# Performance work log

Measured on AMD Instinct MI355X. Metric: run time of the kernel, lower is better.

Reference implementation:

```python
import jax, jax.numpy as jnp
import numpy as np

RES = 7          # pooler resolution
RATIO = 2        # sampling ratio
LEVEL_STRIDES = (4, 8, 16, 32)
NUM_CLASSES = 4
BINS = 8
EPS = 1e-5


def roi_align_one(feat, boxes, scale):
    """feat: [C,H,W]; boxes: [N,4] (t,l,b,r) in image coords. Returns [N,C,RES,RES]."""
    C, H, W = feat.shape
    P = RES * RATIO
    t = boxes[:, 0] * scale - 0.5
    l = boxes[:, 1] * scale - 0.5
    b = boxes[:, 2] * scale - 0.5
    r = boxes[:, 3] * scale - 0.5
    bin_h = (b - t) / RES
    bin_w = (r - l) / RES
    grid = (jnp.arange(P, dtype=feat.dtype) + 0.5) / RATIO      # [P] bin-unit offsets
    ys = jnp.clip(t[:, None] + bin_h[:, None] * grid, 0.0, H - 1.0)  # [N,P]
    xs = jnp.clip(l[:, None] + bin_w[:, None] * grid, 0.0, W - 1.0)  # [N,P]
    y0 = jnp.floor(ys).astype(jnp.int32)
    x0 = jnp.floor(xs).astype(jnp.int32)
    y1 = jnp.minimum(y0 + 1, H - 1)
    x1 = jnp.minimum(x0 + 1, W - 1)
    wy = (ys - y0.astype(feat.dtype))[:, :, None]   # [N,P,1]
    wx = (xs - x0.astype(feat.dtype))[:, None, :]   # [N,1,P]

    def g(yi, xi):  # -> [C,N,P,P]
        return feat[:, yi[:, :, None], xi[:, None, :]]

    v = (g(y0, x0) * (1 - wy) * (1 - wx) + g(y0, x1) * (1 - wy) * wx
         + g(y1, x0) * wy * (1 - wx) + g(y1, x1) * wy * wx)      # [C,N,P,P]
    v = v.reshape(C, -1, RES, RATIO, RES, RATIO).mean(axis=(3, 5))  # avg-pool bins
    return jnp.transpose(v, (1, 0, 2, 3))


def setup_inputs():
    key = jax.random.key(0)
    ks = jax.random.split(key, 16)
    B, N, C, FC = 2, 256, 256, 1024
    f0 = jax.random.normal(ks[0], (B, C, 128, 128), jnp.float32)
    f1 = jax.random.normal(ks[1], (B, C, 64, 64), jnp.float32)
    f2 = jax.random.normal(ks[2], (B, C, 32, 32), jnp.float32)
    f3 = jax.random.normal(ks[3], (B, C, 16, 16), jnp.float32)
    yx = jax.random.uniform(ks[4], (B, N, 2), jnp.float32) * 384.0 + 64.0
    hw = jax.random.uniform(ks[5], (B, N, 2), jnp.float32) * 96.0 + 32.0
    bbox2d = jnp.concatenate([yx, hw], axis=-1)            # yxhw
    anchor_id = jax.random.randint(ks[6], (B, N, 1), 0, 12, jnp.int32)
    zeropad = (jax.random.uniform(ks[7], (B, N, 1)) > 0.1).astype(jnp.float32)
    in_dim = C * RES * RES
    fc1_w = jax.random.normal(ks[8], (FC, in_dim), jnp.float32) / np.sqrt(in_dim)
    fc2_w = jax.random.normal(ks[9], (FC, FC), jnp.float32) / np.sqrt(FC)
    out_ch = NUM_CLASSES * (1 + 6 + 2 * BINS) + 1           # 93
    pred_w = jax.random.normal(ks[10], (out_ch, FC), jnp.float32) * 0.01
    return dict(f0=f0, f1=f1, f2=f2, f3=f3, bbox2d=bbox2d, anchor_id=anchor_id,
                zeropad=zeropad,
                fc1_w=fc1_w, fc1_b=jnp.zeros((FC,)), bn1_g=jnp.ones((FC,)), bn1_b=jnp.zeros((FC,)),
                fc2_w=fc2_w, fc2_b=jnp.zeros((FC,)), bn2_g=jnp.ones((FC,)), bn2_b=jnp.zeros((FC,)),
                pred_w=pred_w, pred_b=jnp.zeros((out_ch,)))


def reference(f0, f1, f2, f3, bbox2d, anchor_id, zeropad,
              fc1_w, fc1_b, bn1_g, bn1_b, fc2_w, fc2_b, bn2_g, bn2_b, pred_w, pred_b):
    feats = [f0, f1, f2, f3]
    B, N, _ = bbox2d.shape
    y, x, h, w = [bbox2d[..., i] for i in range(4)]
    tlbr = jnp.stack([y - h / 2, x - w / 2, y + h / 2, x + w / 2], axis=-1)  # [B,N,4]
    level = anchor_id[..., 0] // 3                                          # [B,N]

    # Route each proposal to its FPN level: compute roi-align per level, select by mask.
    pooled = 0.0
    for i, stride in enumerate(LEVEL_STRIDES):
        roi = jax.vmap(lambda f, bx, s=stride: roi_align_one(f, bx, 1.0 / s))(feats[i], tlbr)  # [B,N,C,R,R]
        mask = (level == i).astype(roi.dtype)[..., None, None, None]
        pooled = pooled + roi * mask

    xflat = pooled.reshape(B * N, -1)
    for w_, b_, g_, be_ in [(fc1_w, fc1_b, bn1_g, bn1_b), (fc2_w, fc2_b, bn2_g, bn2_b)]:
        xflat = xflat @ w_.T + b_
        mu = xflat.mean(axis=0)
        var = xflat.var(axis=0)
        xflat = (xflat - mu) * jax.lax.rsqrt(var + EPS) * g_ + be_   # BatchNorm1d (train mode)
        xflat = jax.nn.relu(xflat)
    pred = (xflat @ pred_w.T + pred_b).reshape(B, N, -1) * zeropad    # [B,N,93]
    strides = level.astype(pred.dtype)[..., None] * zeropad           # [B,N,1]

    # decode: slice per-loss channels (category: NC+1; others: NC*dims)
    ctgr_logit = pred[..., 0:NUM_CLASSES + 1]                                  # [B,N,5]
    d3 = pred[..., 5:5 + NUM_CLASSES * 6].reshape(B, N, NUM_CLASSES, 6)
    o = 5 + NUM_CLASSES * 6
    yaw_cls = pred[..., o:o + NUM_CLASSES * BINS].reshape(B, N, NUM_CLASSES, BINS)
    o += NUM_CLASSES * BINS
    yaw_res = pred[..., o:o + NUM_CLASSES * BINS].reshape(B, N, NUM_CLASSES, BINS)

    # apply 3d box deltas per class (vectorized over class dim)
    anc = bbox2d[:, :, None, :]                     # [B,N,1,4] yxhw
    st = 4.0 * jnp.exp2(strides)                    # [B,N,1] anchor stride in px
    cy = anc[..., 0] + d3[..., 0] * anc[..., 2]
    cx = anc[..., 1] + d3[..., 1] * anc[..., 3]
    nh = anc[..., 2] * jnp.exp(d3[..., 2])
    nw = anc[..., 3] * jnp.exp(d3[..., 3])
    z = d3[..., 4] * st
    ln = jnp.exp(d3[..., 5]) * st
    bbox3d = jnp.stack([cy, cx, z, nh, nw, ln], axis=-1)  # [B,N,NC,6]

    out = jnp.concatenate([
        bbox3d.reshape(B, N, -1),                         # 24
        jax.nn.softmax(ctgr_logit, axis=-1),              # 5
        jax.nn.softmax(yaw_cls, axis=-1).reshape(B, N, -1),  # 32
        (jax.nn.sigmoid(yaw_res) * 0.6 - 0.3).reshape(B, N, -1),  # 32
    ], axis=-1)                                           # [B,N,93]
    return out
```

## Files before the change

kernel.cpp:

```cpp
#include <hip/hip_runtime.h>
#include <cstdint>
#include <cstddef>

typedef __attribute__((ext_vector_type(8))) short bf16x8;
typedef __attribute__((ext_vector_type(4))) float f32x4;
typedef __attribute__((ext_vector_type(4))) int   i32x4;

#define C_CH   256
#define NBOX   512
#define FCDIM  1024
#define K1     12544
#define OUTC   93

__device__ __forceinline__ unsigned short f2bf(float f) {
    unsigned u = __float_as_uint(f);
    u += 0x7fffu + ((u >> 16) & 1u);
    return (unsigned short)(u >> 16);
}
__device__ __forceinline__ float bf2f(short s) {
    return __uint_as_float((unsigned)(unsigned short)s << 16);
}

__global__ __launch_bounds__(256) void cast_bf16_kernel(
    const float* __restrict__ in, short* __restrict__ out, int n8)
{
    int i = blockIdx.x * 256 + threadIdx.x;
    if (i >= n8) return;
    const float4* p = (const float4*)(in + (size_t)i * 8);
    float4 a = p[0], b = p[1];
    union { unsigned short s[8]; i32x4 v; } u;
    u.s[0] = f2bf(a.x); u.s[1] = f2bf(a.y); u.s[2] = f2bf(a.z); u.s[3] = f2bf(a.w);
    u.s[4] = f2bf(b.x); u.s[5] = f2bf(b.y); u.s[6] = f2bf(b.z); u.s[7] = f2bf(b.w);
    *(i32x4*)(out + (size_t)i * 8) = u.v;
}

__global__ __launch_bounds__(256) void transpose_cl_kernel(
    const float* __restrict__ in, short* __restrict__ out, int HW)
{
    __shared__ short tile[128 * 66];
    int p0 = blockIdx.x * 128;
    int c0 = blockIdx.y * 64;
    int b  = blockIdx.z;
    const float* src = in + ((size_t)b * C_CH + c0) * HW + p0;
    int t = threadIdx.x;
    #pragma unroll
    for (int it = 0; it < 16; ++it) {
        int slot = it * 256 + t;
        int cl = slot >> 6;
        int pp = slot & 63;
        float2 v = *(const float2*)(src + (size_t)cl * HW + pp * 2);
        tile[(pp * 2) * 66 + cl]     = (short)f2bf(v.x);
        tile[(pp * 2 + 1) * 66 + cl] = (short)f2bf(v.y);
    }
    __syncthreads();
    short* dst = out + ((size_t)b * HW + p0) * C_CH + c0;
    #pragma unroll
    for (int it = 0; it < 16; ++it) {
        int pl = it * 8 + (t >> 5);
        int c2 = (t & 31) * 2;
        *(unsigned*)(dst + (size_t)pl * C_CH + c2) = *(const unsigned*)&tile[pl * 66 + c2];
    }
}

__global__ __launch_bounds__(512) void roi_kernel(
    const short* __restrict__ g0, const short* __restrict__ g1,
    const short* __restrict__ g2, const short* __restrict__ g3,
    const float* __restrict__ bbox, const int* __restrict__ aid,
    short* __restrict__ pooled)
{
    int bn  = blockIdx.x;
    int b   = bn >> 8;
    int t   = threadIdx.x;
    int c   = t & 255;
    int sub = t >> 8;

    __shared__ int   xo0[14], xo1[14];
    __shared__ float wxs[14];
    __shared__ int   yo0[14], yo1[14];
    __shared__ float wys[14];
    __shared__ short otile[K1];

    float yb = bbox[bn*4+0], xb = bbox[bn*4+1], hb = bbox[bn*4+2], wb = bbox[bn*4+3];
    int level = aid[bn] / 3;
    const short* gsrc = (level == 0) ? g0 : (level == 1) ? g1 : (level == 2) ? g2 : g3;
    int H = 128 >> level;
    float scale = 1.0f / (float)(4 << level);
    const short* gp = gsrc + (size_t)b * H * H * C_CH;

    if (t < 14) {
        float g  = ((float)t + 0.5f) * 0.5f;
        float l0 = (xb - 0.5f*wb) * scale - 0.5f;
        float bw = wb * scale * (1.0f/7.0f);
        float v  = fminf(fmaxf(l0 + bw * g, 0.0f), (float)(H-1));
        int i0 = (int)v;
        xo0[t] = i0 * C_CH;
        xo1[t] = min(i0 + 1, H - 1) * C_CH;
        wxs[t] = v - (float)i0;
    } else if (t < 28) {
        int sy = t - 14;
        float g  = ((float)sy + 0.5f) * 0.5f;
        float t0 = (yb - 0.5f*hb) * scale - 0.5f;
        float bh = hb * scale * (1.0f/7.0f);
        float v  = fminf(fmaxf(t0 + bh * g, 0.0f), (float)(H-1));
        int i0 = (int)v;
        yo0[sy] = i0 * H * C_CH;
        yo1[sy] = min(i0 + 1, H - 1) * H * C_CH;
        wys[sy] = v - (float)i0;
    }
    __syncthreads();

    #pragma unroll 2
    for (int s = sub; s < 49; s += 2) {
        int py = s / 7, px = s - py * 7;
        float acc = 0.0f;
        #pragma unroll
        for (int i = 0; i < 2; i++) {
            int sy = 2 * py + i;
            int ry0 = yo0[sy], ry1 = yo1[sy];
            float wy = wys[sy];
            #pragma unroll
            for (int j = 0; j < 2; j++) {
                int sx = 2 * px + j;
                int cx0 = xo0[sx] + c, cx1 = xo1[sx] + c;
                float wx = wxs[sx];
                float v00 = bf2f(gp[ry0 + cx0]);
                float v01 = bf2f(gp[ry0 + cx1]);
                float v10 = bf2f(gp[ry1 + cx0]);
                float v11 = bf2f(gp[ry1 + cx1]);
                float top = v00 * (1.0f - wx) + v01 * wx;
                float bot = v10 * (1.0f - wx) + v11 * wx;
                acc += top * (1.0f - wy) + bot * wy;
            }
        }
        otile[c * 49 + s] = (short)f2bf(acc * 0.25f);
    }
    __syncthreads();

    const i32x4* srcv = (const i32x4*)otile;
    i32x4* dstv = (i32x4*)(pooled + (size_t)bn * K1);
    for (int j = t; j < (K1 * 2) / 16; j += 512)
        dstv[j] = srcv[j];
}

__global__ __launch_bounds__(256) void gemm_mfma(
    const short* __restrict__ A, const short* __restrict__ Bt,
    float* __restrict__ part, int K, int KC)
{
    __shared__ short As[128 * 32];
    __shared__ short Bs[128 * 32];
    int t = threadIdx.x, lane = t & 63, w = t >> 6;
    int m0 = blockIdx.y * 128, n0 = blockIdx.x * 128;
    size_t k0 = (size_t)blockIdx.z * KC;

    int srow = t >> 1, scol = (t & 1) * 16;
    const short* pa = A  + (size_t)(m0 + srow) * K + scol + k0;
    const short* pb = Bt + (size_t)(n0 + srow) * K + scol + k0;
    short* wa = &As[srow * 32 + scol];
    short* wb = &Bs[srow * 32 + scol];

    int wr = (w >> 1) * 64, wc = (w & 1) * 64;
    int fr = lane & 15, kg = lane >> 4;
    const short* raf = &As[(wr + fr) * 32 + kg * 8];
    const short* rbf = &Bs[(wc + fr) * 32 + kg * 8];

    int nsteps = KC >> 5;
    i32x4 rA0 = *(const i32x4*)pa, rA1 = *(const i32x4*)(pa + 8);
    i32x4 rB0 = *(const i32x4*)pb, rB1 = *(const i32x4*)(pb + 8);

    f32x4 acc[4][4] = {};
    for (int s = 0; s < nsteps; ++s) {
        *(i32x4*)wa = rA0; *(i32x4*)(wa + 8) = rA1;
        *(i32x4*)wb = rB0; *(i32x4*)(wb + 8) = rB1;
        __syncthreads();
        if (s + 1 < nsteps) {
            const short* na = pa + (size_t)(s + 1) * 32;
            const short* nb = pb + (size_t)(s + 1) * 32;
            rA0 = *(const i32x4*)na; rA1 = *(const i32x4*)(na + 8);
            rB0 = *(const i32x4*)nb; rB1 = *(const i32x4*)(nb + 8);
        }
        bf16x8 af[4], bm[4];
        #pragma unroll
        for (int i = 0; i < 4; i++) af[i] = *(const bf16x8*)(raf + i * 16 * 32);
        #pragma unroll
        for (int j = 0; j < 4; j++) bm[j] = *(const bf16x8*)(rbf + j * 16 * 32);
        #pragma unroll
        for (int i = 0; i < 4; i++)
            #pragma unroll
            for (int j = 0; j < 4; j++)
                acc[i][j] = __builtin_amdgcn_mfma_f32_16x16x32_bf16(af[i], bm[j], acc[i][j], 0, 0, 0);
        __syncthreads();
    }

    float* base = part + (size_t)blockIdx.z * NBOX * FCDIM;
    #pragma unroll
    for (int i = 0; i < 4; i++)
        #pragma unroll
        for (int j = 0; j < 4; j++)
            #pragma unroll
            for (int r = 0; r < 4; r++) {
                int row = m0 + wr + i * 16 + kg * 4 + r;
                int col = n0 + wc + j * 16 + fr;
                base[(size_t)row * FCDIM + col] = acc[i][j][r];
            }
}

template<int NZ>
__global__ __launch_bounds__(256) void bn_stats1(
    const float* __restrict__ part, float* __restrict__ xsum, float* __restrict__ pstat)
{
    int tc = threadIdx.x & 63;
    int tr = threadIdx.x >> 6;
    int c  = blockIdx.x * 64 + tc;
    int r0 = blockIdx.y * 32;
    const size_t P = (size_t)NBOX * FCDIM;

    float s = 0.0f, q = 0.0f;
    #pragma unroll
    for (int rr = 0; rr < 8; rr++) {
        size_t o = (size_t)(r0 + tr + rr * 4) * FCDIM + c;
        float x = 0.0f;
        #pragma unroll
        for (int z = 0; z < NZ; z++) x += part[o + (size_t)z * P];
        xsum[o] = x;
        s += x; q += x * x;
    }
    __shared__ float Ss[4][64], Sq[4][64];
    Ss[tr][tc] = s; Sq[tr][tc] = q;
    __syncthreads();
    if (tr == 0) {
        float S = Ss[0][tc] + Ss[1][tc] + Ss[2][tc] + Ss[3][tc];
        float Q = Sq[0][tc] + Sq[1][tc] + Sq[2][tc] + Sq[3][tc];
        pstat[blockIdx.y * FCDIM + c] = S;
        pstat[16 * FCDIM + blockIdx.y * FCDIM + c] = Q;
    }
}

__global__ __launch_bounds__(256) void bn_stats2(
    const float* __restrict__ pstat, const float* __restrict__ g,
    const float* __restrict__ be, float* __restrict__ scsh)
{
    int c = blockIdx.x * 256 + threadIdx.x;
    float S = 0.0f, Q = 0.0f;
    #pragma unroll
    for (int i = 0; i < 16; i++) {
        S += pstat[i * FCDIM + c];
        Q += pstat[16 * FCDIM + i * FCDIM + c];
    }
    float mu  = S * (1.0f / NBOX);
    float var = Q * (1.0f / NBOX) - mu * mu;
    float a = g[c] * rsqrtf(var + 1e-5f);
    scsh[c]         = a;
    scsh[FCDIM + c] = be[c] - mu * a;
}

template<bool BF>
__global__ __launch_bounds__(256) void bn_apply(
    const float* __restrict__ xsum, const float* __restrict__ scsh,
    short* __restrict__ obf, float* __restrict__ of)
{
    size_t base = ((size_t)blockIdx.x * 256 + threadIdx.x) * 8;
    int c0 = (int)(base & (FCDIM - 1));
    float4 x0 = *(const float4*)(xsum + base);
    float4 x1 = *(const float4*)(xsum + base + 4);
    float4 a0 = *(const float4*)(scsh + c0);
    float4 a1 = *(const float4*)(scsh + c0 + 4);
    float4 b0 = *(const float4*)(scsh + FCDIM + c0);
    float4 b1 = *(const float4*)(scsh + FCDIM + c0 + 4);
    float r[8];
    r[0] = fmaxf(x0.x*a0.x + b0.x, 0.0f);
    r[1] = fmaxf(x0.y*a0.y + b0.y, 0.0f);
    r[2] = fmaxf(x0.z*a0.z + b0.z, 0.0f);
    r[3] = fmaxf(x0.w*a0.w + b0.w, 0.0f);
    r[4] = fmaxf(x1.x*a1.x + b1.x, 0.0f);
    r[5] = fmaxf(x1.y*a1.y + b1.y, 0.0f);
    r[6] = fmaxf(x1.z*a1.z + b1.z, 0.0f);
    r[7] = fmaxf(x1.w*a1.w + b1.w, 0.0f);
    if (BF) {
        union { unsigned short s[8]; i32x4 v; } u;
        #pragma unroll
        for (int i = 0; i < 8; i++) u.s[i] = f2bf(r[i]);
        *(i32x4*)(obf + base) = u.v;
    } else {
        *(float4*)(of + base)     = *(float4*)&r[0];
        *(float4*)(of + base + 4) = *(float4*)&r[4];
    }
}

__global__ __launch_bounds__(128) void pred_kernel(
    const float* __restrict__ xin, const float* __restrict__ pw,
    const float* __restrict__ pb, const float* __restrict__ bbox,
    const int* __restrict__ aid, const float* __restrict__ zp,
    float* __restrict__ out)
{
    int bn = blockIdx.x;
    int t  = threadIdx.x;
    __shared__ float xs[FCDIM];
    __shared__ float pr[OUTC];
    for (int i = t; i < FCDIM; i += 128)
        xs[i] = xin[(size_t)bn * FCDIM + i];
    __syncthreads();

    float z = zp[bn];
    if (t < OUTC) {
        const float* wrow = pw + (size_t)t * FCDIM;
        float acc = 0.0f;
        for (int k = 0; k < FCDIM; k += 4) {
            float4 w4 = *(const float4*)(wrow + k);
            acc += xs[k] * w4.x + xs[k+1] * w4.y + xs[k+2] * w4.z + xs[k+3] * w4.w;
        }
        pr[t] = (acc + pb[t]) * z;
    }
    __syncthreads();

    if (t < OUTC) {
        float y = bbox[bn*4+0], x = bbox[bn*4+1], h = bbox[bn*4+2], w = bbox[bn*4+3];
        int lvl = aid[bn] / 3;
        float st = 4.0f * exp2f((float)lvl * z);
        float o;
        if (t < 24) {
            int k = t / 6, j = t - k * 6;
            const float* d = &pr[5 + k * 6];
            switch (j) {
                case 0:  o = y + d[0] * h;  break;
                case 1:  o = x + d[1] * w;  break;
                case 2:  o = d[4] * st;     break;
                case 3:  o = h * expf(d[2]); break;
                case 4:  o = w * expf(d[3]); break;
                default: o = expf(d[5]) * st; break;
            }
        } else if (t < 29) {
            float m = pr[0];
            #pragma unroll
            for (int i = 1; i < 5; i++) m = fmaxf(m, pr[i]);
            float den = 0.0f;
            #pragma unroll
            for (int i = 0; i < 5; i++) den += expf(pr[i] - m);
            o = expf(pr[t - 24] - m) / den;
        } else if (t < 61) {
            int i = t - 29, k = i >> 3;
            const float* qq = &pr[29 + k * 8];
            float m = qq[0];
            #pragma unroll
            for (int ii = 1; ii < 8; ii++) m = fmaxf(m, qq[ii]);
            float den = 0.0f;
            #pragma unroll
            for (int ii = 0; ii < 8; ii++) den += expf(qq[ii] - m);
            o = expf(pr[t] - m) / den;
        } else {
            o = 1.0f / (1.0f + expf(-pr[t])) * 0.6f - 0.3f;
        }
        out[(size_t)bn * OUTC + t] = o;
    }
}

extern "C" void kernel_launch(void* const* d_in, const int* in_sizes, int n_in,
                              void* d_out, int out_size, void* d_ws, size_t ws_size,
                              hipStream_t stream)
{
    const float* f0   = (const float*)d_in[0];
    const float* f1   = (const float*)d_in[1];
    const float* f2   = (const float*)d_in[2];
    const float* f3   = (const float*)d_in[3];
    const float* bbox = (const float*)d_in[4];
    const int*   aid  = (const int*)d_in[5];
    const float* zp   = (const float*)d_in[6];
    const float* fc1w = (const float*)d_in[7];
    const float* bn1g = (const float*)d_in[9];
    const float* bn1b = (const float*)d_in[10];
    const float* fc2w = (const float*)d_in[11];
    const float* bn2g = (const float*)d_in[13];
    const float* bn2b = (const float*)d_in[14];
    const float* pw   = (const float*)d_in[15];
    const float* pb   = (const float*)d_in[16];
    float* out = (float*)d_out;

    char* ws = (char*)d_ws;
    short* pooled = (short*)(ws);
    float* xsum   = (float*)(ws);
    short* x1n    = (short*)(ws + 2097152);
    short* w2     = (short*)(ws + 3145728);
    float* x2n    = (float*)(ws + 5242880);
    short* gt0    = (short*)(ws + 12845056);
    short* gt1    = (short*)(ws + 29622272);
    short* gt2    = (short*)(ws + 33816576);
    short* gt3    = (short*)(ws + 34865152);
    short* w1     = (short*)(ws + 12845056);
    float* part2  = (float*)(ws + 12845056);
    float* part1  = (float*)(ws + 38535168);
    float* pstat  = (float*)(ws + 53215232);
    float* scsh   = (float*)(ws + 53346304);

    transpose_cl_kernel<<<dim3(128, 4, 2), 256, 0, stream>>>(f0, gt0, 16384);
    transpose_cl_kernel<<<dim3( 32, 4, 2), 256, 0, stream>>>(f1, gt1,  4096);
    transpose_cl_kernel<<<dim3(  8, 4, 2), 256, 0, stream>>>(f2, gt2,  1024);
    transpose_cl_kernel<<<dim3(  2, 4, 2), 256, 0, stream>>>(f3, gt3,   256);

    roi_kernel<<<NBOX, 512, 0, stream>>>(gt0, gt1, gt2, gt3, bbox, aid, pooled);

    cast_bf16_kernel<<<(K1 * FCDIM / 8 + 255) / 256, 256, 0, stream>>>(fc1w, w1, K1 * FCDIM / 8);

    dim3 g1(FCDIM / 128, NBOX / 128, 7);
    gemm_mfma<<<g1, 256, 0, stream>>>(pooled, w1, part1, K1, K1 / 7);

    cast_bf16_kernel<<<(FCDIM * FCDIM / 8 + 255) / 256, 256, 0, stream>>>(fc2w, w2, FCDIM * FCDIM / 8);

    bn_stats1<7><<<dim3(16, 16), 256, 0, stream>>>(part1, xsum, pstat);
    bn_stats2<<<4, 256, 0, stream>>>(pstat, bn1g, bn1b, scsh);
    bn_apply<true><<<256, 256, 0, stream>>>(xsum, scsh, x1n, nullptr);

    dim3 g2(FCDIM / 128, NBOX / 128, 8);
    gemm_mfma<<<g2, 256, 0, stream>>>(x1n, w2, part2, FCDIM, FCDIM / 8);

    bn_stats1<8><<<dim3(16, 16), 256, 0, stream>>>(part2, xsum, pstat);
    bn_stats2<<<4, 256, 0, stream>>>(pstat, bn2g, bn2b, scsh);
    bn_apply<false><<<256, 256, 0, stream>>>(xsum, scsh, nullptr, x2n);

    pred_kernel<<<NBOX, 128, 0, stream>>>(x2n, pw, pb, bbox, aid, zp, out);
}
```

Measured before the change: 152.5 us.

## Fuse fc1 weight cast into GEMM, merge transposes, retile fc1 to 256x256

Removes the separate fp32-to-bf16 cast pass over the large fc1 weight: a new fc1 GEMM reads fp32 weights directly and converts them to bf16 while staging into shared memory. It uses 256x256 tiles with 512 threads and split-K 14, replacing 128x128 tiles with split-K 7. The four per-level feature transposes are merged into one launch, and the workspace is re-laid out so the buffers no longer alias. The cost is twice the bytes read for the weight inside the GEMM, in-loop conversion work, higher register pressure from 32 accumulators per thread, and a larger split-K partial buffer for the BN stats to reduce.

```diff
diff --git a/kernel.cpp b/kernel.cpp
--- a/kernel.cpp
+++ b/kernel.cpp
@@ -11,6 +11,8 @@
 #define FCDIM  1024
 #define K1     12544
 #define OUTC   93
+#define Z1     14
+#define Z2     8
 
 __device__ __forceinline__ unsigned short f2bf(float f) {
     unsigned u = __float_as_uint(f);
@@ -34,31 +36,41 @@
     *(i32x4*)(out + (size_t)i * 8) = u.v;
 }
 
-__global__ __launch_bounds__(256) void transpose_cl_kernel(
-    const float* __restrict__ in, short* __restrict__ out, int HW)
+__global__ __launch_bounds__(256) void transpose_all_kernel(
+    const float* __restrict__ f0, const float* __restrict__ f1,
+    const float* __restrict__ f2, const float* __restrict__ f3,
+    short* __restrict__ g0, short* __restrict__ g1,
+    short* __restrict__ g2, short* __restrict__ g3)
 {
     __shared__ short tile[128 * 66];
-    int p0 = blockIdx.x * 128;
-    int c0 = blockIdx.y * 64;
-    int b  = blockIdx.z;
-    const float* src = in + ((size_t)b * C_CH + c0) * HW + p0;
+    int id = blockIdx.x;
+    const float* src; short* dst; int HW, nx;
+    if (id < 1024)      { src = f0; dst = g0; HW = 16384; nx = 128; }
+    else if (id < 1280) { id -= 1024; src = f1; dst = g1; HW = 4096; nx = 32; }
+    else if (id < 1344) { id -= 1280; src = f2; dst = g2; HW = 1024; nx = 8; }
+    else                { id -= 1344; src = f3; dst = g3; HW = 256;  nx = 2; }
+    int xb = id % nx;  int rest = id / nx;
+    int cy = rest & 3; int b = rest >> 2;
+    int p0 = xb * 128, c0 = cy * 64;
+
+    const float* s = src + ((size_t)b * C_CH + c0) * HW + p0;
     int t = threadIdx.x;
     #pragma unroll
     for (int it = 0; it < 16; ++it) {
         int slot = it * 256 + t;
         int cl = slot >> 6;
         int pp = slot & 63;
-        float2 v = *(const float2*)(src + (size_t)cl * HW + pp * 2);
+        float2 v = *(const float2*)(s + (size_t)cl * HW + pp * 2);
         tile[(pp * 2) * 66 + cl]     = (short)f2bf(v.x);
         tile[(pp * 2 + 1) * 66 + cl] = (short)f2bf(v.y);
     }
     __syncthreads();
-    short* dst = out + ((size_t)b * HW + p0) * C_CH + c0;
+    short* d = dst + ((size_t)b * HW + p0) * C_CH + c0;
     #pragma unroll
     for (int it = 0; it < 16; ++it) {
         int pl = it * 8 + (t >> 5);
         int c2 = (t & 31) * 2;
-        *(unsigned*)(dst + (size_t)pl * C_CH + c2) = *(const unsigned*)&tile[pl * 66 + c2];
+        *(unsigned*)(d + (size_t)pl * C_CH + c2) = *(const unsigned*)&tile[pl * 66 + c2];
     }
 }
 
@@ -142,6 +154,75 @@
         dstv[j] = srcv[j];
 }
 
+__global__ __launch_bounds__(512, 2) void gemm_fc1(
+    const short* __restrict__ A, const float* __restrict__ Bw,
+    float* __restrict__ part, int K, int KC)
+{
+    __shared__ short As[256 * 32];
+    __shared__ short Bs[256 * 32];
+    int t = threadIdx.x, lane = t & 63, w = t >> 6;
+    int n0 = blockIdx.x * 256, m0 = blockIdx.y * 256;
+    size_t k0 = (size_t)blockIdx.z * KC;
+
+    int srow = t >> 1, scol = (t & 1) * 16;
+    const short* pa  = A  + (size_t)(m0 + srow) * K + scol + k0;
+    const float* pbw = Bw + (size_t)(n0 + srow) * K + scol + k0;
+    short* wa = &As[srow * 32 + scol];
+    short* wb = &Bs[srow * 32 + scol];
+
+    int wr = (w >> 2) * 128, wc = (w & 3) * 64;
+    int fr = lane & 15, kg = lane >> 4;
+    const short* raf = &As[(wr + fr) * 32 + kg * 8];
+    const short* rbf = &Bs[(wc + fr) * 32 + kg * 8];
+
+    int nsteps = KC >> 5;
+    i32x4  rA0 = *(const i32x4*)pa,        rA1 = *(const i32x4*)(pa + 8);
+    float4 rB0 = *(const float4*)pbw,      rB1 = *(const float4*)(pbw + 4);
+    float4 rB2 = *(const float4*)(pbw + 8), rB3 = *(const float4*)(pbw + 12);
+
+    f32x4 acc[8][4] = {};
+    for (int s = 0; s < nsteps; ++s) {
+        union { unsigned short us[16]; i32x4 v[2]; } ub;
+        ub.us[0]  = f2bf(rB0.x); ub.us[1]  = f2bf(rB0.y); ub.us[2]  = f2bf(rB0.z); ub.us[3]  = f2bf(rB0.w);
+        ub.us[4]  = f2bf(rB1.x); ub.us[5]  = f2bf(rB1.y); ub.us[6]  = f2bf(rB1.z); ub.us[7]  = f2bf(rB1.w);
+        ub.us[8]  = f2bf(rB2.x); ub.us[9]  = f2bf(rB2.y); ub.us[10] = f2bf(rB2.z); ub.us[11] = f2bf(rB2.w);
+        ub.us[12] = f2bf(rB3.x); ub.us[13] = f2bf(rB3.y); ub.us[14] = f2bf(rB3.z); ub.us[15] = f2bf(rB3.w);
+        *(i32x4*)wa = rA0;     *(i32x4*)(wa + 8) = rA1;
+        *(i32x4*)wb = ub.v[0]; *(i32x4*)(wb + 8) = ub.v[1];
+        __syncthreads();
+        if (s + 1 < nsteps) {
+            const short* na = pa  + (size_t)(s + 1) * 32;
+            const float* nb = pbw + (size_t)(s + 1) * 32;
+            rA0 = *(const i32x4*)na;       rA1 = *(const i32x4*)(na + 8);
+            rB0 = *(const float4*)nb;      rB1 = *(const float4*)(nb + 4);
+            rB2 = *(const float4*)(nb + 8); rB3 = *(const float4*)(nb + 12);
+        }
+        bf16x8 af[8], bm[4];
+        #pragma unroll
+        for (int i = 0; i < 8; i++) af[i] = *(const bf16x8*)(raf + i * 16 * 32);
+        #pragma unroll
+        for (int j = 0; j < 4; j++) bm[j] = *(const bf16x8*)(rbf + j * 16 * 32);
+        #pragma unroll
+        for (int i = 0; i < 8; i++)
+            #pragma unroll
+            for (int j = 0; j < 4; j++)
+                acc[i][j] = __builtin_amdgcn_mfma_f32_16x16x32_bf16(af[i], bm[j], acc[i][j], 0, 0, 0);
+        __syncthreads();
+    }
+
+    float* base = part + (size_t)blockIdx.z * NBOX * FCDIM;
+    #pragma unroll
+    for (int i = 0; i < 8; i++)
+        #pragma unroll
+        for (int j = 0; j < 4; j++)
+            #pragma unroll
+            for (int r = 0; r < 4; r++) {
+                int row = m0 + wr + i * 16 + kg * 4 + r;
+                int col = n0 + wc + j * 16 + fr;
+                base[(size_t)row * FCDIM + col] = acc[i][j][r];
+            }
+}
+
 __global__ __launch_bounds__(256) void gemm_mfma(
     const short* __restrict__ A, const short* __restrict__ Bt,
     float* __restrict__ part, int K, int KC)
@@ -376,42 +457,36 @@
 
     char* ws = (char*)d_ws;
     short* pooled = (short*)(ws);
-    float* xsum   = (float*)(ws);
-    short* x1n    = (short*)(ws + 2097152);
-    short* w2     = (short*)(ws + 3145728);
-    float* x2n    = (float*)(ws + 5242880);
-    short* gt0    = (short*)(ws + 12845056);
-    short* gt1    = (short*)(ws + 29622272);
-    short* gt2    = (short*)(ws + 33816576);
-    short* gt3    = (short*)(ws + 34865152);
-    short* w1     = (short*)(ws + 12845056);
-    float* part2  = (float*)(ws + 12845056);
-    float* part1  = (float*)(ws + 38535168);
-    float* pstat  = (float*)(ws + 53215232);
-    float* scsh   = (float*)(ws + 53346304);
-
-    transpose_cl_kernel<<<dim3(128, 4, 2), 256, 0, stream>>>(f0, gt0, 16384);
-    transpose_cl_kernel<<<dim3( 32, 4, 2), 256, 0, stream>>>(f1, gt1,  4096);
-    transpose_cl_kernel<<<dim3(  8, 4, 2), 256, 0, stream>>>(f2, gt2,  1024);
-    transpose_cl_kernel<<<dim3(  2, 4, 2), 256, 0, stream>>>(f3, gt3,   256);
+    short* gt0    = (short*)(ws + 13631488);
+    short* gt1    = (short*)(ws + 30408704);
+    short* gt2    = (short*)(ws + 34603008);
+    short* gt3    = (short*)(ws + 35651584);
+    short* w2     = (short*)(ws + 36700160);
+    float* part1  = (float*)(ws + 40894464);
+    float* part2  = (float*)(ws + 71303168);
+    float* xsum   = (float*)(ws + 89128960);
+    short* x1n    = (short*)(ws + 91226112);
+    float* x2n    = (float*)(ws + 92274688);
+    float* pstat  = (float*)(ws + 94371840);
+    float* scsh   = (float*)(ws + 94502912);
+
+    transpose_all_kernel<<<1360, 256, 0, stream>>>(f0, f1, f2, f3, gt0, gt1, gt2, gt3);
 
     roi_kernel<<<NBOX, 512, 0, stream>>>(gt0, gt1, gt2, gt3, bbox, aid, pooled);
 
-    cast_bf16_kernel<<<(K1 * FCDIM / 8 + 255) / 256, 256, 0, stream>>>(fc1w, w1, K1 * FCDIM / 8);
-
-    dim3 g1(FCDIM / 128, NBOX / 128, 7);
-    gemm_mfma<<<g1, 256, 0, stream>>>(pooled, w1, part1, K1, K1 / 7);
+    dim3 g1(FCDIM / 256, NBOX / 256, Z1);
+    gemm_fc1<<<g1, 512, 0, stream>>>(pooled, fc1w, part1, K1, K1 / Z1);
 
     cast_bf16_kernel<<<(FCDIM * FCDIM / 8 + 255) / 256, 256, 0, stream>>>(fc2w, w2, FCDIM * FCDIM / 8);
 
-    bn_stats1<7><<<dim3(16, 16), 256, 0, stream>>>(part1, xsum, pstat);
+    bn_stats1<Z1><<<dim3(16, 16), 256, 0, stream>>>(part1, xsum, pstat);
     bn_stats2<<<4, 256, 0, stream>>>(pstat, bn1g, bn1b, scsh);
     bn_apply<true><<<256, 256, 0, stream>>>(xsum, scsh, x1n, nullptr);
 
-    dim3 g2(FCDIM / 128, NBOX / 128, 8);
-    gemm_mfma<<<g2, 256, 0, stream>>>(x1n, w2, part2, FCDIM, FCDIM / 8);
-
-    bn_stats1<8><<<dim3(16, 16), 256, 0, stream>>>(part2, xsum, pstat);
+    dim3 g2(FCDIM / 128, NBOX / 128, Z2);
+    gemm_mfma<<<g2, 256, 0, stream>>>(x1n, w2, part2, FCDIM, FCDIM / Z2);
+
+    bn_stats1<Z2><<<dim3(16, 16), 256, 0, stream>>>(part2, xsum, pstat);
     bn_stats2<<<4, 256, 0, stream>>>(pstat, bn2g, bn2b, scsh);
     bn_apply<false><<<256, 256, 0, stream>>>(xsum, scsh, nullptr, x2n);
 
```

After: 154.6 us. About the same (+1.4%).

## Double-buffer GEMM via direct global-to-LDS loads, merge transposes, deepen split-K

Applied to the files above, without the earlier changes.

Replaces the register-staged GEMM with a double-buffered version that uses global_load_lds to copy tiles straight into shared memory while the current tile feeds MFMA. FC1 split-K grows from 7 to 14 slices for more blocks, and blocks are indexed linearly so that blocks with the same row tile run together. The four per-level transpose launches are merged into one launch, and the workspace is re-laid out so buffers no longer alias. In exchange, more split-K partials must be written and reduced, and the workspace footprint is larger.

```diff
diff --git a/kernel.cpp b/kernel.cpp
--- a/kernel.cpp
+++ b/kernel.cpp
@@ -11,6 +11,8 @@
 #define FCDIM  1024
 #define K1     12544
 #define OUTC   93
+#define Z1     14
+#define Z2     8
 
 __device__ __forceinline__ unsigned short f2bf(float f) {
     unsigned u = __float_as_uint(f);
@@ -19,6 +21,11 @@
 }
 __device__ __forceinline__ float bf2f(short s) {
     return __uint_as_float((unsigned)(unsigned short)s << 16);
+}
+__device__ __forceinline__ void stage16(const short* g, const short* l) {
+    __builtin_amdgcn_global_load_lds(
+        (const __attribute__((address_space(1))) void*)g,
+        (__attribute__((address_space(3))) void*)l, 16, 0, 0);
 }
 
 __global__ __launch_bounds__(256) void cast_bf16_kernel(
@@ -34,31 +41,41 @@
     *(i32x4*)(out + (size_t)i * 8) = u.v;
 }
 
-__global__ __launch_bounds__(256) void transpose_cl_kernel(
-    const float* __restrict__ in, short* __restrict__ out, int HW)
+__global__ __launch_bounds__(256) void transpose_all_kernel(
+    const float* __restrict__ f0, const float* __restrict__ f1,
+    const float* __restrict__ f2, const float* __restrict__ f3,
+    short* __restrict__ g0, short* __restrict__ g1,
+    short* __restrict__ g2, short* __restrict__ g3)
 {
     __shared__ short tile[128 * 66];
-    int p0 = blockIdx.x * 128;
-    int c0 = blockIdx.y * 64;
-    int b  = blockIdx.z;
-    const float* src = in + ((size_t)b * C_CH + c0) * HW + p0;
+    int id = blockIdx.x;
+    const float* src; short* dst; int HW, nx;
+    if (id < 1024)      { src = f0; dst = g0; HW = 16384; nx = 128; }
+    else if (id < 1280) { id -= 1024; src = f1; dst = g1; HW = 4096; nx = 32; }
+    else if (id < 1344) { id -= 1280; src = f2; dst = g2; HW = 1024; nx = 8; }
+    else                { id -= 1344; src = f3; dst = g3; HW = 256;  nx = 2; }
+    int xb = id % nx;  int rest = id / nx;
+    int cy = rest & 3; int b = rest >> 2;
+    int p0 = xb * 128, c0 = cy * 64;
+
+    const float* s = src + ((size_t)b * C_CH + c0) * HW + p0;
     int t = threadIdx.x;
     #pragma unroll
     for (int it = 0; it < 16; ++it) {
         int slot = it * 256 + t;
         int cl = slot >> 6;
         int pp = slot & 63;
-        float2 v = *(const float2*)(src + (size_t)cl * HW + pp * 2);
+        float2 v = *(const float2*)(s + (size_t)cl * HW + pp * 2);
         tile[(pp * 2) * 66 + cl]     = (short)f2bf(v.x);
         tile[(pp * 2 + 1) * 66 + cl] = (short)f2bf(v.y);
     }
     __syncthreads();
-    short* dst = out + ((size_t)b * HW + p0) * C_CH + c0;
+    short* d = dst + ((size_t)b * HW + p0) * C_CH + c0;
     #pragma unroll
     for (int it = 0; it < 16; ++it) {
         int pl = it * 8 + (t >> 5);
         int c2 = (t & 31) * 2;
-        *(unsigned*)(dst + (size_t)pl * C_CH + c2) = *(const unsigned*)&tile[pl * 66 + c2];
+        *(unsigned*)(d + (size_t)pl * C_CH + c2) = *(const unsigned*)&tile[pl * 66 + c2];
     }
 }
 
@@ -142,47 +159,60 @@
         dstv[j] = srcv[j];
 }
 
-__global__ __launch_bounds__(256) void gemm_mfma(
+__global__ __launch_bounds__(256) void gemm_db(
     const short* __restrict__ A, const short* __restrict__ Bt,
-    float* __restrict__ part, int K, int KC)
-{
-    __shared__ short As[128 * 32];
-    __shared__ short Bs[128 * 32];
+    float* __restrict__ part, int K, int KC, int NP)
+{
+    __shared__ short As[2][4096];
+    __shared__ short Bs[2][4096];
     int t = threadIdx.x, lane = t & 63, w = t >> 6;
-    int m0 = blockIdx.y * 128, n0 = blockIdx.x * 128;
-    size_t k0 = (size_t)blockIdx.z * KC;
-
-    int srow = t >> 1, scol = (t & 1) * 16;
-    const short* pa = A  + (size_t)(m0 + srow) * K + scol + k0;
-    const short* pb = Bt + (size_t)(n0 + srow) * K + scol + k0;
-    short* wa = &As[srow * 32 + scol];
-    short* wb = &Bs[srow * 32 + scol];
+    int bid = blockIdx.x;
+    int p = bid % NP, m = bid / NP;
+    int n = p & 7, z = p >> 3;
+    int m0 = m * 128, n0 = n * 128;
+    size_t k0 = (size_t)z * KC;
+
+    int gslot = (lane & 3) * 8;
+    int lrow  = lane >> 2;
+    int qa0 = 2 * w, qa1 = 2 * w + 1;
+    const short* gA0 = A  + (size_t)(m0 + qa0 * 16 + lrow) * K + k0 + gslot;
+    const short* gA1 = A  + (size_t)(m0 + qa1 * 16 + lrow) * K + k0 + gslot;
+    const short* gB0 = Bt + (size_t)(n0 + qa0 * 16 + lrow) * K + k0 + gslot;
+    const short* gB1 = Bt + (size_t)(n0 + qa1 * 16 + lrow) * K + k0 + gslot;
+    const short* lA0 = &As[0][qa0 * 512];
+    const short* lA1 = &As[0][qa1 * 512];
+    const short* lB0 = &Bs[0][qa0 * 512];
+    const short* lB1 = &Bs[0][qa1 * 512];
 
     int wr = (w >> 1) * 64, wc = (w & 1) * 64;
     int fr = lane & 15, kg = lane >> 4;
-    const short* raf = &As[(wr + fr) * 32 + kg * 8];
-    const short* rbf = &Bs[(wc + fr) * 32 + kg * 8];
+    int raoff = (wr + fr) * 32 + kg * 8;
+    int rboff = (wc + fr) * 32 + kg * 8;
 
     int nsteps = KC >> 5;
-    i32x4 rA0 = *(const i32x4*)pa, rA1 = *(const i32x4*)(pa + 8);
-    i32x4 rB0 = *(const i32x4*)pb, rB1 = *(const i32x4*)(pb + 8);
+
+    stage16(gA0, lA0); stage16(gA1, lA1);
+    stage16(gB0, lB0); stage16(gB1, lB1);
+    __syncthreads();
 
     f32x4 acc[4][4] = {};
     for (int s = 0; s < nsteps; ++s) {
-        *(i32x4*)wa = rA0; *(i32x4*)(wa + 8) = rA1;
-        *(i32x4*)wb = rB0; *(i32x4*)(wb + 8) = rB1;
-        __syncthreads();
+        int cur = s & 1;
         if (s + 1 < nsteps) {
-            const short* na = pa + (size_t)(s + 1) * 32;
-            const short* nb = pb + (size_t)(s + 1) * 32;
-            rA0 = *(const i32x4*)na; rA1 = *(const i32x4*)(na + 8);
-            rB0 = *(const i32x4*)nb; rB1 = *(const i32x4*)(nb + 8);
+            int nxt = cur ^ 1;
+            int ks = (s + 1) * 32;
+            stage16(gA0 + ks, lA0 + nxt * 4096);
+            stage16(gA1 + ks, lA1 + nxt * 4096);
+            stage16(gB0 + ks, lB0 + nxt * 4096);
+            stage16(gB1 + ks, lB1 + nxt * 4096);
         }
+        const short* ra = &As[cur][raoff];
+        const short* rb = &Bs[cur][rboff];
         bf16x8 af[4], bm[4];
         #pragma unroll
-        for (int i = 0; i < 4; i++) af[i] = *(const bf16x8*)(raf + i * 16 * 32);
-        #pragma unroll
-        for (int j = 0; j < 4; j++) bm[j] = *(const bf16x8*)(rbf + j * 16 * 32);
+        for (int i = 0; i < 4; i++) af[i] = *(const bf16x8*)(ra + i * 512);
+        #pragma unroll
+        for (int j = 0; j < 4; j++) bm[j] = *(const bf16x8*)(rb + j * 512);
         #pragma unroll
         for (int i = 0; i < 4; i++)
             #pragma unroll
@@ -191,7 +221,7 @@
         __syncthreads();
     }
 
-    float* base = part + (size_t)blockIdx.z * NBOX * FCDIM;
+    float* base = part + (size_t)z * NBOX * FCDIM;
     #pragma unroll
     for (int i = 0; i < 4; i++)
         #pragma unroll
@@ -376,42 +406,37 @@
 
     char* ws = (char*)d_ws;
     short* pooled = (short*)(ws);
-    float* xsum   = (float*)(ws);
-    short* x1n    = (short*)(ws + 2097152);
-    short* w2     = (short*)(ws + 3145728);
-    float* x2n    = (float*)(ws + 5242880);
-    short* gt0    = (short*)(ws + 12845056);
-    short* gt1    = (short*)(ws + 29622272);
-    short* gt2    = (short*)(ws + 33816576);
-    short* gt3    = (short*)(ws + 34865152);
-    short* w1     = (short*)(ws + 12845056);
-    float* part2  = (float*)(ws + 12845056);
-    float* part1  = (float*)(ws + 38535168);
-    float* pstat  = (float*)(ws + 53215232);
-    float* scsh   = (float*)(ws + 53346304);
-
-    transpose_cl_kernel<<<dim3(128, 4, 2), 256, 0, stream>>>(f0, gt0, 16384);
-    transpose_cl_kernel<<<dim3( 32, 4, 2), 256, 0, stream>>>(f1, gt1,  4096);
-    transpose_cl_kernel<<<dim3(  8, 4, 2), 256, 0, stream>>>(f2, gt2,  1024);
-    transpose_cl_kernel<<<dim3(  2, 4, 2), 256, 0, stream>>>(f3, gt3,   256);
+    short* gt0    = (short*)(ws + 13631488);
+    short* gt1    = (short*)(ws + 30408704);
+    short* gt2    = (short*)(ws + 34603008);
+    short* gt3    = (short*)(ws + 35651584);
+    short* w1     = (short*)(ws + 36700160);
+    short* w2     = (short*)(ws + 62390272);
+    float* part1  = (float*)(ws + 64487424);
+    float* part2  = (float*)(ws + 123207680);
+    float* xsum   = (float*)(ws + 139984896);
+    short* x1n    = (short*)(ws + 142082048);
+    float* x2n    = (float*)(ws + 143130624);
+    float* pstat  = (float*)(ws + 145227776);
+    float* scsh   = (float*)(ws + 145358848);
+
+    transpose_all_kernel<<<1360, 256, 0, stream>>>(f0, f1, f2, f3, gt0, gt1, gt2, gt3);
 
     roi_kernel<<<NBOX, 512, 0, stream>>>(gt0, gt1, gt2, gt3, bbox, aid, pooled);
 
     cast_bf16_kernel<<<(K1 * FCDIM / 8 + 255) / 256, 256, 0, stream>>>(fc1w, w1, K1 * FCDIM / 8);
 
-    dim3 g1(FCDIM / 128, NBOX / 128, 7);
-    gemm_mfma<<<g1, 256, 0, stream>>>(pooled, w1, part1, K1, K1 / 7);
+    gemm_db<<<4 * 8 * Z1, 256, 0, stream>>>(pooled, w1, part1, K1, K1 / Z1, 8 * Z1);
 
     cast_bf16_kernel<<<(FCDIM * FCDIM / 8 + 255) / 256, 256, 0, stream>>>(fc2w, w2, FCDIM * FCDIM / 8);
 
-    bn_stats1<7><<<dim3(16, 16), 256, 0, stream>>>(part1, xsum, pstat);
+    bn_stats1<Z1><<<dim3(16, 16), 256, 0, stream>>>(part1, xsum, pstat);
     bn_stats2<<<4, 256, 0, stream>>>(pstat, bn1g, bn1b, scsh);
     bn_apply<true><<<256, 256, 0, stream>>>(xsum, scsh, x1n, nullptr);
 
-    dim3 g2(FCDIM / 128, NBOX / 128, 8);
-    gemm_mfma<<<g2, 256, 0, stream>>>(x1n, w2, part2, FCDIM, FCDIM / 8);
-
-    bn_stats1<8><<<dim3(16, 16), 256, 0, stream>>>(part2, xsum, pstat);
+    gemm_db<<<4 * 8 * Z2, 256, 0, stream>>>(x1n, w2, part2, FCDIM, FCDIM / Z2, 8 * Z2);
+
+    bn_stats1<Z2><<<dim3(16, 16), 256, 0, stream>>>(part2, xsum, pstat);
     bn_stats2<<<4, 256, 0, stream>>>(pstat, bn2g, bn2b, scsh);
     bn_apply<false><<<256, 256, 0, stream>>>(xsum, scsh, nullptr, x2n);
 
```

Result: faster. 138.4 us (-9.2%).
